# Optimization experiments

Measured on AMD Instinct MI355X. Metric: run time of the kernel, lower is better.

## Reference

```python
import jax, jax.numpy as jnp
import numpy as np

N = 50000      # nodes
E = 800000     # edges (avg degree 16)
D_IN = 32      # raw feature dim
D = 96         # hidden == out dim (residual requires equality)
L = 4          # number of GatedGCN layers
NC = 10        # n_classes
EPS = 1e-6


def _w(k, shape, fan_in):
    return jax.random.normal(k, shape, jnp.float32) / np.sqrt(fan_in).astype(np.float32)


def setup_inputs() -> dict:
    key = jax.random.key(0)
    ks = jax.random.split(key, 16)
    inp = {
        'h': jax.random.normal(ks[0], (N, D_IN), jnp.float32),
        'e': jax.random.normal(ks[1], (E, D_IN), jnp.float32),
        'src': jax.random.randint(ks[2], (E,), 0, N, jnp.int32),
        'dst': jax.random.randint(ks[3], (E,), 0, N, jnp.int32),
        'fp_w': _w(ks[4], (D_IN, D), D_IN), 'fp_b': jnp.zeros((D,), jnp.float32),
        'ep_w': _w(ks[5], (D_IN, D), D_IN), 'ep_b': jnp.zeros((D,), jnp.float32),
    }
    for i, name in enumerate(['A', 'B', 'C', 'D', 'E']):
        inp[name + '_w'] = _w(ks[6 + i], (L, D, D), D)
        inp[name + '_b'] = jnp.zeros((L, D), jnp.float32)
    inp['mlp0_w'] = _w(ks[11], (D, D // 2), D); inp['mlp0_b'] = jnp.zeros((D // 2,), jnp.float32)
    inp['mlp1_w'] = _w(ks[12], (D // 2, D // 4), D // 2); inp['mlp1_b'] = jnp.zeros((D // 4,), jnp.float32)
    inp['mlp2_w'] = _w(ks[13], (D // 4, NC), D // 4); inp['mlp2_b'] = jnp.zeros((NC,), jnp.float32)
    return inp


def reference(h, e, src, dst, fp_w, fp_b, ep_w, ep_b,
              A_w, A_b, B_w, B_b, C_w, C_b, D_w, D_b, E_w, E_b,
              mlp0_w, mlp0_b, mlp1_w, mlp1_b, mlp2_w, mlp2_b):
    # input projections
    h = h @ fp_w + fp_b                       # [N, D]
    e = e @ ep_w + ep_b                       # [E, D]

    def layer(carry, p):
        h, e = carry
        Aw, Ab, Bw, Bb, Cw, Cb, Dw, Db, Ew, Eb = p
        Ah = h @ Aw + Ab
        Bh = h @ Bw + Bb
        Ce = e @ Cw + Cb
        Dh = h @ Dw + Db
        Eh = h @ Ew + Eb
        # edge gate: e_ij = D h_i + E h_j + C e_ij  (u_add_v with u=src, v=dst)
        e_new = Dh[src] + Eh[dst] + Ce          # [E, D]
        sigma = jax.nn.sigmoid(e_new)           # [E, D]
        # gated aggregation to destination nodes
        num = jax.ops.segment_sum(Bh[src] * sigma, dst, num_segments=N)  # [N, D]
        den = jax.ops.segment_sum(sigma, dst, num_segments=N)            # [N, D]
        h_new = Ah + num / (den + EPS)
        # relu then residual (batch_norm=False, dropout eval no-op)
        return (h + jax.nn.relu(h_new), e + jax.nn.relu(e_new)), None

    (h, e), _ = jax.lax.scan(layer, (h, e),
                             (A_w, A_b, B_w, B_b, C_w, C_b, D_w, D_b, E_w, E_b))

    # MLPReadout (L=2 halvings) + sigmoid head
    y = jax.nn.relu(h @ mlp0_w + mlp0_b)
    y = jax.nn.relu(y @ mlp1_w + mlp1_b)
    y = y @ mlp2_w + mlp2_b
    return jax.nn.sigmoid(y)                    # [N, NC]
```

## Files before the change

kernel.cpp:

```cpp
#include <hip/hip_runtime.h>

#define NN 50000
#define NE 800000
#define DIN 32
#define DD 96
#define NL 4
#define NCLS 10
#define EPSF 1e-6f

typedef unsigned short u16;
typedef unsigned int u32;

typedef __bf16 bf16x8 __attribute__((ext_vector_type(8)));
typedef float f32x4 __attribute__((ext_vector_type(4)));

static __device__ __forceinline__ float bf2f(u16 u) {
    return __uint_as_float(((u32)u) << 16);
}
static __device__ __forceinline__ u16 f2bf(float f) {
    u32 x = __float_as_uint(f);
    x += 0x7FFFu + ((x >> 16) & 1u);
    return (u16)(x >> 16);
}
static __device__ __forceinline__ u32 pk2(float a, float b) {
    return (u32)f2bf(a) | ((u32)f2bf(b) << 16);
}
static __device__ __forceinline__ float unlo(u32 u) { return __uint_as_float(u << 16); }
static __device__ __forceinline__ float unhi(u32 u) { return __uint_as_float(u & 0xFFFF0000u); }

__global__ void k_zero_i(int* __restrict__ p, int n) {
    int i = blockIdx.x * blockDim.x + threadIdx.x;
    if (i < n) p[i] = 0;
}

__global__ void k_hist(const int* __restrict__ dst, int* __restrict__ counts) {
    int i = blockIdx.x * blockDim.x + threadIdx.x;
    if (i < NE) atomicAdd(&counts[dst[i]], 1);
}

__global__ __launch_bounds__(1024) void k_scan(const int* __restrict__ counts,
                                               int* __restrict__ row_ptr,
                                               int* __restrict__ cursor, int n) {
    __shared__ int wsum[16];
    __shared__ int carry_s;
    const int tid = threadIdx.x;
    const int lane = tid & 63, wid = tid >> 6;
    if (tid == 0) carry_s = 0;
    __syncthreads();
    for (int base = 0; base < n; base += 1024) {
        int i = base + tid;
        int v = (i < n) ? counts[i] : 0;
        int x = v;
#pragma unroll
        for (int off = 1; off < 64; off <<= 1) {
            int t = __shfl_up(x, (unsigned)off, 64);
            if (lane >= off) x += t;
        }
        if (lane == 63) wsum[wid] = x;
        __syncthreads();
        if (wid == 0 && lane < 16) {
            int s = wsum[lane];
#pragma unroll
            for (int off = 1; off < 16; off <<= 1) {
                int t = __shfl_up(s, (unsigned)off, 16);
                if (lane >= off) s += t;
            }
            wsum[lane] = s;
        }
        __syncthreads();
        int wbase = (wid > 0) ? wsum[wid - 1] : 0;
        int carry = carry_s;
        int excl = carry + wbase + x - v;
        if (i < n) { row_ptr[i] = excl; cursor[i] = excl; }
        __syncthreads();
        if (tid == 0) carry_s = carry + wsum[15];
        __syncthreads();
    }
    if (tid == 0) row_ptr[n] = carry_s;
}

__global__ void k_scatter(const int* __restrict__ src, const int* __restrict__ dst,
                          int* __restrict__ cursor, int* __restrict__ eperm,
                          int* __restrict__ srcp) {
    int i = blockIdx.x * blockDim.x + threadIdx.x;
    if (i >= NE) return;
    int pos = atomicAdd(&cursor[dst[i]], 1);
    eperm[pos] = i;
    srcp[pos] = src[i];
}

__global__ void k_packCw(const float* __restrict__ W_all, u16* __restrict__ wf, int kperm) {
    int q = blockIdx.x * blockDim.x + threadIdx.x;
    if (q >= NL * 6 * 3 * 64) return;
    int l = q / (6 * 3 * 64);
    int rem = q - l * (6 * 3 * 64);
    int tile = rem / (3 * 64);
    int rem2 = rem - tile * (3 * 64);
    int c = rem2 >> 6, lane = rem2 & 63;
    const float* W = W_all + (long)l * DD * DD;
    int n = tile * 16 + (lane & 15);
    int k0 = c * 32 + (lane >> 4) * 8;
    u16 w[8];
#pragma unroll
    for (int j = 0; j < 8; ++j) {
        int kk = k0 + j;
        int kact = kperm ? ((kk % 6) * 16 + kk / 6) : kk;
        w[j] = f2bf(W[kact * DD + n]);
    }
    *(uint4*)&wf[(long)q * 8] = *(uint4*)w;
}

__global__ void k_packW32(const float* __restrict__ W, u16* __restrict__ wf) {
    int q = blockIdx.x * blockDim.x + threadIdx.x;
    if (q >= 6 * 64) return;
    int tile = q >> 6, lane = q & 63;
    int n = tile * 16 + (lane & 15);
    int k0 = (lane >> 4) * 8;
    u16 w[8];
#pragma unroll
    for (int j = 0; j < 8; ++j) w[j] = f2bf(W[(k0 + j) * DD + n]);
    *(uint4*)&wf[q * 8] = *(uint4*)w;
}

template <bool BFOUT, bool PERM, bool POUT>
__global__ __launch_bounds__(256) void k_proj_m(const float* __restrict__ X,
                                                const u16* __restrict__ wf,
                                                const float* __restrict__ B,
                                                void* __restrict__ Y,
                                                const int* __restrict__ eperm,
                                                int ntiles) {
    const int lane = threadIdx.x & 63;
    const int gw = (blockIdx.x * blockDim.x + threadIdx.x) >> 6;
    const int nw = (gridDim.x * blockDim.x) >> 6;
    const int lm = lane & 15, quad = lane >> 4;

    bf16x8 bfr[6];
    float bias[6];
#pragma unroll
    for (int t = 0; t < 6; ++t) {
        bfr[t] = *(const bf16x8*)&wf[(t * 64 + lane) * 8];
        bias[t] = B[t * 16 + lm];
    }

    for (int tile = gw; tile < ntiles; tile += nw) {
        const int row = tile * 16 + lm;
        const long srow = PERM ? (long)eperm[row] : (long)row;
        float4 x0 = *(const float4*)&X[srow * DIN + quad * 8];
        float4 x1 = *(const float4*)&X[srow * DIN + quad * 8 + 4];
        u32 ap[4] = {pk2(x0.x, x0.y), pk2(x0.z, x0.w), pk2(x1.x, x1.y), pk2(x1.z, x1.w)};
        bf16x8 af = *(bf16x8*)ap;
        f32x4 acc[6];
#pragma unroll
        for (int t = 0; t < 6; ++t) {
            acc[t] = (f32x4){0.f, 0.f, 0.f, 0.f};
            acc[t] = __builtin_amdgcn_mfma_f32_16x16x32_bf16(af, bfr[t], acc[t], 0, 0, 0);
        }
        const long rbase = (long)tile * 16 + quad * 4;
        if (POUT) {
#pragma unroll
            for (int r = 0; r < 4; ++r) {
                u16* p = (u16*)Y + (rbase + r) * DD + lm * 6;
                *(u32*)p       = pk2(acc[0][r] + bias[0], acc[1][r] + bias[1]);
                *(u32*)(p + 2) = pk2(acc[2][r] + bias[2], acc[3][r] + bias[3]);
                *(u32*)(p + 4) = pk2(acc[4][r] + bias[4], acc[5][r] + bias[5]);
            }
        } else {
#pragma unroll
            for (int t = 0; t < 6; ++t) {
                const int j = t * 16 + lm;
#pragma unroll
                for (int r = 0; r < 4; ++r) {
                    float v = acc[t][r] + bias[t];
                    if (BFOUT) ((u16*)Y)[(rbase + r) * DD + j] = f2bf(v);
                    else       ((float*)Y)[(rbase + r) * DD + j] = v;
                }
            }
        }
    }
}

__global__ __launch_bounds__(256) void k_gemm4m(const float* __restrict__ X,
                                                const u16* __restrict__ awf, const float* __restrict__ ab,
                                                const u16* __restrict__ bwf, const float* __restrict__ bb,
                                                const u16* __restrict__ dwf, const float* __restrict__ db,
                                                const u16* __restrict__ ewf, const float* __restrict__ eb,
                                                float* __restrict__ Y0, u16* __restrict__ Y1,
                                                u16* __restrict__ Y2, u16* __restrict__ Y3,
                                                int ntiles) {
    const int lane = threadIdx.x & 63;
    const int w = threadIdx.x >> 6;
    const int lm = lane & 15, quad = lane >> 4;
    const u16* wf = (w == 0) ? awf : (w == 1) ? bwf : (w == 2) ? dwf : ewf;
    const float* bp = (w == 0) ? ab : (w == 1) ? bb : (w == 2) ? db : eb;

    bf16x8 bfr[6][3];
    float bias[6];
#pragma unroll
    for (int t = 0; t < 6; ++t) {
#pragma unroll
        for (int c = 0; c < 3; ++c)
            bfr[t][c] = *(const bf16x8*)&wf[((t * 3 + c) * 64 + lane) * 8];
        bias[t] = bp[t * 16 + lm];
    }

    for (int tile = blockIdx.x; tile < ntiles; tile += gridDim.x) {
        const float* xr = X + (long)(tile * 16 + lm) * DD;
        bf16x8 a[3];
#pragma unroll
        for (int c = 0; c < 3; ++c) {
            float4 x0 = *(const float4*)&xr[c * 32 + quad * 8];
            float4 x1 = *(const float4*)&xr[c * 32 + quad * 8 + 4];
            u32 ap[4] = {pk2(x0.x, x0.y), pk2(x0.z, x0.w), pk2(x1.x, x1.y), pk2(x1.z, x1.w)};
            a[c] = *(bf16x8*)ap;
        }
        f32x4 acc[6];
#pragma unroll
        for (int t = 0; t < 6; ++t) {
            acc[t] = (f32x4){0.f, 0.f, 0.f, 0.f};
#pragma unroll
            for (int c = 0; c < 3; ++c)
                acc[t] = __builtin_amdgcn_mfma_f32_16x16x32_bf16(a[c], bfr[t][c], acc[t], 0, 0, 0);
        }
        const long rbase = (long)tile * 16 + quad * 4;
        if (w == 0) {
#pragma unroll
            for (int t = 0; t < 6; ++t) {
                const int j = t * 16 + lm;
#pragma unroll
                for (int r = 0; r < 4; ++r) Y0[(rbase + r) * DD + j] = acc[t][r] + bias[t];
            }
        } else {
            u16* Yp = (w == 1) ? Y1 : (w == 2) ? Y2 : Y3;
#pragma unroll
            for (int r = 0; r < 4; ++r) {
                u16* p = Yp + (rbase + r) * DD + lm * 6;
                *(u32*)p       = pk2(acc[0][r] + bias[0], acc[1][r] + bias[1]);
                *(u32*)(p + 2) = pk2(acc[2][r] + bias[2], acc[3][r] + bias[3]);
                *(u32*)(p + 4) = pk2(acc[4][r] + bias[4], acc[5][r] + bias[5]);
            }
        }
    }
}

__global__ __launch_bounds__(256) void k_node_edge_w(u16* ebuf,
                                                     const u16* __restrict__ cwf,
                                                     const float* __restrict__ Cb,
                                                     const u16* __restrict__ Dh,
                                                     const u16* __restrict__ Eh,
                                                     const u16* __restrict__ Bh,
                                                     const int* __restrict__ srcp,
                                                     const int* __restrict__ row_ptr,
                                                     const float* __restrict__ Ah,
                                                     float* __restrict__ hbuf) {
    const int lane = threadIdx.x & 63;
    const int gw = (blockIdx.x * blockDim.x + threadIdx.x) >> 6;
    const int nw = (gridDim.x * blockDim.x) >> 6;
    const int lm = lane & 15, quad = lane >> 4;

    bf16x8 bfrag[6][3];
    float cb[6];
#pragma unroll
    for (int t = 0; t < 6; ++t) {
#pragma unroll
        for (int c = 0; c < 3; ++c)
            bfrag[t][c] = *(const bf16x8*)&cwf[((t * 3 + c) * 64 + lane) * 8];
        cb[t] = Cb[t * 16 + lm];
    }

    for (int n = gw; n < NN; n += nw) {
        const int r0 = row_ptr[n], r1 = row_ptr[n + 1];
        float eh[6];
        {
            const u16* ep = Eh + (long)n * DD + lm * 6;
            u32 e0 = *(const u32*)ep, e1 = *(const u32*)(ep + 2), e2 = *(const u32*)(ep + 4);
            eh[0] = unlo(e0); eh[1] = unhi(e0); eh[2] = unlo(e1);
            eh[3] = unhi(e1); eh[4] = unlo(e2); eh[5] = unhi(e2);
        }
        float nacc[6] = {0.f, 0.f, 0.f, 0.f, 0.f, 0.f};
        float dacc[6] = {0.f, 0.f, 0.f, 0.f, 0.f, 0.f};

        for (int chunk = r0; chunk < r1; chunk += 16) {
            const int rows = r1 - chunk < 16 ? r1 - chunk : 16;
            const long arow = chunk + (lm < rows ? lm : 0);
            bf16x8 a[3];
#pragma unroll
            for (int c = 0; c < 3; ++c)
                a[c] = *(const bf16x8*)&ebuf[arow * DD + c * 32 + quad * 8];
            int sr[4];
#pragma unroll
            for (int r = 0; r < 4; ++r) {
                int rl = quad * 4 + r;
                sr[r] = (chunk + rl < r1) ? srcp[chunk + rl] : 0;
            }
            f32x4 acc[6];
#pragma unroll
            for (int t = 0; t < 6; ++t) {
                acc[t] = (f32x4){0.f, 0.f, 0.f, 0.f};
#pragma unroll
                for (int c = 0; c < 3; ++c)
                    acc[t] = __builtin_amdgcn_mfma_f32_16x16x32_bf16(a[c], bfrag[t][c], acc[t], 0, 0, 0);
            }
#pragma unroll
            for (int r = 0; r < 4; ++r) {
                const int rl = quad * 4 + r;
                if (rl < rows) {
                    const long s = sr[r];
                    const u16* dp = Dh + s * DD + lm * 6;
                    const u16* bp = Bh + s * DD + lm * 6;
                    u16* ep = ebuf + (long)(chunk + rl) * DD + lm * 6;
                    u32 d0 = *(const u32*)dp, d1 = *(const u32*)(dp + 2), d2 = *(const u32*)(dp + 4);
                    u32 b0 = *(const u32*)bp, b1 = *(const u32*)(bp + 2), b2 = *(const u32*)(bp + 4);
                    u32 o0 = *(const u32*)ep, o1 = *(const u32*)(ep + 2), o2 = *(const u32*)(ep + 4);
                    float dh[6] = {unlo(d0), unhi(d0), unlo(d1), unhi(d1), unlo(d2), unhi(d2)};
                    float bh[6] = {unlo(b0), unhi(b0), unlo(b1), unhi(b1), unlo(b2), unhi(b2)};
                    float od[6] = {unlo(o0), unhi(o0), unlo(o1), unhi(o1), unlo(o2), unhi(o2)};
                    float ov[6];
#pragma unroll
                    for (int t = 0; t < 6; ++t) {
                        float en = acc[t][r] + cb[t] + dh[t] + eh[t];
                        float sg = 1.f / (1.f + __expf(-en));
                        nacc[t] += bh[t] * sg;
                        dacc[t] += sg;
                        ov[t] = od[t] + fmaxf(en, 0.f);
                    }
                    *(u32*)ep       = pk2(ov[0], ov[1]);
                    *(u32*)(ep + 2) = pk2(ov[2], ov[3]);
                    *(u32*)(ep + 4) = pk2(ov[4], ov[5]);
                }
            }
        }
#pragma unroll
        for (int t = 0; t < 6; ++t) {
            float x = nacc[t], y = dacc[t];
            x += __shfl_xor(x, 16); y += __shfl_xor(y, 16);
            x += __shfl_xor(x, 32); y += __shfl_xor(y, 32);
            nacc[t] = x; dacc[t] = y;
        }
        if (quad == 0) {
#pragma unroll
            for (int t = 0; t < 6; ++t) {
                const int j = t * 16 + lm;
                float val = Ah[(long)n * DD + j] + nacc[t] / (dacc[t] + EPSF);
                hbuf[(long)n * DD + j] += fmaxf(val, 0.f);
            }
        }
    }
}

__global__ void k_mlp(const float* __restrict__ X, const float* __restrict__ W,
                      const float* __restrict__ B, float* __restrict__ Y,
                      int K, int Dout, int act, long total) {
    long idx = (long)blockIdx.x * blockDim.x + threadIdx.x;
    if (idx >= total) return;
    int row = (int)(idx / Dout);
    int j = (int)(idx - (long)row * Dout);
    const float* xr = X + (long)row * K;
    float acc = B[j];
    for (int k = 0; k < K; ++k) acc = fmaf(xr[k], W[k * Dout + j], acc);
    if (act == 1) acc = fmaxf(acc, 0.f);
    else if (act == 2) acc = 1.f / (1.f + __expf(-acc));
    Y[idx] = acc;
}

extern "C" void kernel_launch(void* const* d_in, const int* in_sizes, int n_in,
                              void* d_out, int out_size, void* d_ws, size_t ws_size,
                              hipStream_t stream) {
    const float* h_in = (const float*)d_in[0];
    const float* e_in = (const float*)d_in[1];
    const int* src = (const int*)d_in[2];
    const int* dst = (const int*)d_in[3];
    const float* fp_w = (const float*)d_in[4];
    const float* fp_b = (const float*)d_in[5];
    const float* ep_w = (const float*)d_in[6];
    const float* ep_b = (const float*)d_in[7];
    const float* A_w = (const float*)d_in[8];
    const float* A_b = (const float*)d_in[9];
    const float* B_w = (const float*)d_in[10];
    const float* B_b = (const float*)d_in[11];
    const float* C_w = (const float*)d_in[12];
    const float* C_b = (const float*)d_in[13];
    const float* D_w = (const float*)d_in[14];
    const float* D_b = (const float*)d_in[15];
    const float* E_w = (const float*)d_in[16];
    const float* E_b = (const float*)d_in[17];
    const float* mlp0_w = (const float*)d_in[18];
    const float* mlp0_b = (const float*)d_in[19];
    const float* mlp1_w = (const float*)d_in[20];
    const float* mlp1_b = (const float*)d_in[21];
    const float* mlp2_w = (const float*)d_in[22];
    const float* mlp2_b = (const float*)d_in[23];
    float* out = (float*)d_out;

    const size_t ND = (size_t)NN * DD;
    const size_t ED = (size_t)NE * DD;
    const size_t FRAG = (size_t)NL * 6 * 3 * 64 * 8;
    char* w = (char*)d_ws;
    float* hbuf = (float*)w; w += ND * 4;
    float* Ahb  = (float*)w; w += ND * 4;
    u16* Bhb = (u16*)w; w += ND * 2;
    u16* Dhb = (u16*)w; w += ND * 2;
    u16* Ehb = (u16*)w; w += ND * 2;
    u16* ebuf = (u16*)w; w += ED * 2;
    int* counts  = (int*)w; w += (size_t)NN * 4;
    int* row_ptr = (int*)w; w += (size_t)(NN + 1) * 4 + 12;
    int* cursor  = (int*)w; w += (size_t)NN * 4;
    int* eperm   = (int*)w; w += (size_t)NE * 4;
    int* srcp    = (int*)w; w += (size_t)NE * 4;
    u16* awf = (u16*)w; w += FRAG * 2;
    u16* bwf = (u16*)w; w += FRAG * 2;
    u16* cwf = (u16*)w; w += FRAG * 2;
    u16* dwf = (u16*)w; w += FRAG * 2;
    u16* ewf = (u16*)w; w += FRAG * 2;
    u16* wfp = (u16*)w; w += (size_t)6 * 64 * 8 * 2;
    u16* wep = (u16*)w; w += (size_t)6 * 64 * 8 * 2;
    size_t need = (size_t)(w - (char*)d_ws);
    if (ws_size < need) return;

    k_zero_i<<<(NN + 255) / 256, 256, 0, stream>>>(counts, NN);
    k_hist<<<(NE + 255) / 256, 256, 0, stream>>>(dst, counts);
    k_scan<<<1, 1024, 0, stream>>>(counts, row_ptr, cursor, NN);
    k_scatter<<<(NE + 255) / 256, 256, 0, stream>>>(src, dst, cursor, eperm, srcp);
    const int gPack = (NL * 6 * 3 * 64 + 255) / 256;
    k_packCw<<<gPack, 256, 0, stream>>>(A_w, awf, 0);
    k_packCw<<<gPack, 256, 0, stream>>>(B_w, bwf, 0);
    k_packCw<<<gPack, 256, 0, stream>>>(C_w, cwf, 1);
    k_packCw<<<gPack, 256, 0, stream>>>(D_w, dwf, 0);
    k_packCw<<<gPack, 256, 0, stream>>>(E_w, ewf, 0);
    k_packW32<<<2, 256, 0, stream>>>(fp_w, wfp);
    k_packW32<<<2, 256, 0, stream>>>(ep_w, wep);

    k_proj_m<false, false, false><<<256, 256, 0, stream>>>(h_in, wfp, fp_b, hbuf, nullptr, NN / 16);
    k_proj_m<true, true, true><<<1024, 256, 0, stream>>>(e_in, wep, ep_b, ebuf, eperm, NE / 16);

    const size_t LFRAG = (size_t)6 * 3 * 64 * 8;
    for (int l = 0; l < NL; ++l) {
        const float* Ab = A_b + (size_t)l * DD;
        const float* Bb = B_b + (size_t)l * DD;
        const float* Cb = C_b + (size_t)l * DD;
        const float* Db = D_b + (size_t)l * DD;
        const float* Eb = E_b + (size_t)l * DD;

        k_gemm4m<<<640, 256, 0, stream>>>(hbuf,
                                          awf + l * LFRAG, Ab, bwf + l * LFRAG, Bb,
                                          dwf + l * LFRAG, Db, ewf + l * LFRAG, Eb,
                                          Ahb, Bhb, Dhb, Ehb, NN / 16);
        k_node_edge_w<<<2560, 256, 0, stream>>>(ebuf, cwf + l * LFRAG, Cb, Dhb, Ehb, Bhb,
                                                srcp, row_ptr, Ahb, hbuf);
    }

    float* y1 = Ahb;
    float* y2 = Ahb + (size_t)NN * 48;
    long t0 = (long)NN * 48, t1 = (long)NN * 24, t2 = (long)NN * NCLS;
    k_mlp<<<(int)((t0 + 255) / 256), 256, 0, stream>>>(hbuf, mlp0_w, mlp0_b, y1, DD, 48, 1, t0);
    k_mlp<<<(int)((t1 + 255) / 256), 256, 0, stream>>>(y1, mlp1_w, mlp1_b, y2, 48, 24, 1, t1);
    k_mlp<<<(int)((t2 + 255) / 256), 256, 0, stream>>>(y2, mlp2_w, mlp2_b, out, 24, NCLS, 2, t2);
}
```

Measured before the change: 1.430 ms.

## Split edge work into 16-edge chunks with atomic num/den accumulation

Replaces per-node wave assignment in the edge kernel with a flat list of 16-edge chunks, built once by a second scan over per-node chunk counts. This is meant to fix load imbalance from skewed node degrees. Partial numerator and denominator sums now go to zeroed fp32 buffers through atomicAdd, and a separate combine kernel applies the residual update. In exchange it adds two extra kernels and extra global traffic per layer (zeroing two N×D buffers, atomics, one more pass). The gemm4m grid is also enlarged.

```diff
diff --git a/kernel.cpp b/kernel.cpp
--- a/kernel.cpp
+++ b/kernel.cpp
@@ -33,13 +33,18 @@
     if (i < n) p[i] = 0;
 }
 
+__global__ void k_zero_f4(float4* __restrict__ p, int n4) {
+    int i = blockIdx.x * blockDim.x + threadIdx.x;
+    if (i < n4) p[i] = make_float4(0.f, 0.f, 0.f, 0.f);
+}
+
 __global__ void k_hist(const int* __restrict__ dst, int* __restrict__ counts) {
     int i = blockIdx.x * blockDim.x + threadIdx.x;
     if (i < NE) atomicAdd(&counts[dst[i]], 1);
 }
 
 __global__ __launch_bounds__(1024) void k_scan(const int* __restrict__ counts,
-                                               int* __restrict__ row_ptr,
+                                               int* __restrict__ ptr,
                                                int* __restrict__ cursor, int n) {
     __shared__ int wsum[16];
     __shared__ int carry_s;
@@ -71,12 +76,12 @@
         int wbase = (wid > 0) ? wsum[wid - 1] : 0;
         int carry = carry_s;
         int excl = carry + wbase + x - v;
-        if (i < n) { row_ptr[i] = excl; cursor[i] = excl; }
+        if (i < n) { ptr[i] = excl; cursor[i] = excl; }
         __syncthreads();
         if (tid == 0) carry_s = carry + wsum[15];
         __syncthreads();
     }
-    if (tid == 0) row_ptr[n] = carry_s;
+    if (tid == 0) ptr[n] = carry_s;
 }
 
 __global__ void k_scatter(const int* __restrict__ src, const int* __restrict__ dst,
@@ -87,6 +92,23 @@
     int pos = atomicAdd(&cursor[dst[i]], 1);
     eperm[pos] = i;
     srcp[pos] = src[i];
+}
+
+__global__ void k_chunkcnt(const int* __restrict__ row_ptr, int* __restrict__ counts) {
+    int n = blockIdx.x * blockDim.x + threadIdx.x;
+    if (n < NN) counts[n] = (row_ptr[n + 1] - row_ptr[n] + 15) / 16;
+}
+
+__global__ void k_fillchunk(const int* __restrict__ row_ptr, const int* __restrict__ chunk_ptr,
+                            int* __restrict__ chunk_node, int* __restrict__ chunk_start) {
+    int n = blockIdx.x * blockDim.x + threadIdx.x;
+    if (n >= NN) return;
+    int r0 = row_ptr[n], r1 = row_ptr[n + 1];
+    int base = chunk_ptr[n];
+    for (int c = 0; r0 + 16 * c < r1; ++c) {
+        chunk_node[base + c] = n;
+        chunk_start[base + c] = r0 + 16 * c;
+    }
 }
 
 __global__ void k_packCw(const float* __restrict__ W_all, u16* __restrict__ wf, int kperm) {
@@ -242,16 +264,19 @@
     }
 }
 
-__global__ __launch_bounds__(256) void k_node_edge_w(u16* ebuf,
-                                                     const u16* __restrict__ cwf,
-                                                     const float* __restrict__ Cb,
-                                                     const u16* __restrict__ Dh,
-                                                     const u16* __restrict__ Eh,
-                                                     const u16* __restrict__ Bh,
-                                                     const int* __restrict__ srcp,
-                                                     const int* __restrict__ row_ptr,
-                                                     const float* __restrict__ Ah,
-                                                     float* __restrict__ hbuf) {
+__global__ __launch_bounds__(256) void k_edge_c(u16* ebuf,
+                                                const u16* __restrict__ cwf,
+                                                const float* __restrict__ Cb,
+                                                const u16* __restrict__ Dh,
+                                                const u16* __restrict__ Eh,
+                                                const u16* __restrict__ Bh,
+                                                const int* __restrict__ srcp,
+                                                const int* __restrict__ row_ptr,
+                                                const int* __restrict__ chunk_node,
+                                                const int* __restrict__ chunk_start,
+                                                const int* __restrict__ chunk_total,
+                                                float* __restrict__ num,
+                                                float* __restrict__ den) {
     const int lane = threadIdx.x & 63;
     const int gw = (blockIdx.x * blockDim.x + threadIdx.x) >> 6;
     const int nw = (gridDim.x * blockDim.x) >> 6;
@@ -266,9 +291,12 @@
             bfrag[t][c] = *(const bf16x8*)&cwf[((t * 3 + c) * 64 + lane) * 8];
         cb[t] = Cb[t * 16 + lm];
     }
-
-    for (int n = gw; n < NN; n += nw) {
-        const int r0 = row_ptr[n], r1 = row_ptr[n + 1];
+    const int cnt = *chunk_total;
+
+    for (int ci = gw; ci < cnt; ci += nw) {
+        const int n = chunk_node[ci];
+        const int start = chunk_start[ci];
+        const int rows = min(16, row_ptr[n + 1] - start);
         float eh[6];
         {
             const u16* ep = Eh + (long)n * DD + lm * 6;
@@ -276,57 +304,53 @@
             eh[0] = unlo(e0); eh[1] = unhi(e0); eh[2] = unlo(e1);
             eh[3] = unhi(e1); eh[4] = unlo(e2); eh[5] = unhi(e2);
         }
+        const long arow = start + (lm < rows ? lm : 0);
+        bf16x8 a[3];
+#pragma unroll
+        for (int c = 0; c < 3; ++c)
+            a[c] = *(const bf16x8*)&ebuf[arow * DD + c * 32 + quad * 8];
+        int sr[4];
+#pragma unroll
+        for (int r = 0; r < 4; ++r) {
+            int rl = quad * 4 + r;
+            sr[r] = (rl < rows) ? srcp[start + rl] : 0;
+        }
+        f32x4 acc[6];
+#pragma unroll
+        for (int t = 0; t < 6; ++t) {
+            acc[t] = (f32x4){0.f, 0.f, 0.f, 0.f};
+#pragma unroll
+            for (int c = 0; c < 3; ++c)
+                acc[t] = __builtin_amdgcn_mfma_f32_16x16x32_bf16(a[c], bfrag[t][c], acc[t], 0, 0, 0);
+        }
         float nacc[6] = {0.f, 0.f, 0.f, 0.f, 0.f, 0.f};
         float dacc[6] = {0.f, 0.f, 0.f, 0.f, 0.f, 0.f};
-
-        for (int chunk = r0; chunk < r1; chunk += 16) {
-            const int rows = r1 - chunk < 16 ? r1 - chunk : 16;
-            const long arow = chunk + (lm < rows ? lm : 0);
-            bf16x8 a[3];
-#pragma unroll
-            for (int c = 0; c < 3; ++c)
-                a[c] = *(const bf16x8*)&ebuf[arow * DD + c * 32 + quad * 8];
-            int sr[4];
-#pragma unroll
-            for (int r = 0; r < 4; ++r) {
-                int rl = quad * 4 + r;
-                sr[r] = (chunk + rl < r1) ? srcp[chunk + rl] : 0;
-            }
-            f32x4 acc[6];
-#pragma unroll
-            for (int t = 0; t < 6; ++t) {
-                acc[t] = (f32x4){0.f, 0.f, 0.f, 0.f};
-#pragma unroll
-                for (int c = 0; c < 3; ++c)
-                    acc[t] = __builtin_amdgcn_mfma_f32_16x16x32_bf16(a[c], bfrag[t][c], acc[t], 0, 0, 0);
-            }
-#pragma unroll
-            for (int r = 0; r < 4; ++r) {
-                const int rl = quad * 4 + r;
-                if (rl < rows) {
-                    const long s = sr[r];
-                    const u16* dp = Dh + s * DD + lm * 6;
-                    const u16* bp = Bh + s * DD + lm * 6;
-                    u16* ep = ebuf + (long)(chunk + rl) * DD + lm * 6;
-                    u32 d0 = *(const u32*)dp, d1 = *(const u32*)(dp + 2), d2 = *(const u32*)(dp + 4);
-                    u32 b0 = *(const u32*)bp, b1 = *(const u32*)(bp + 2), b2 = *(const u32*)(bp + 4);
-                    u32 o0 = *(const u32*)ep, o1 = *(const u32*)(ep + 2), o2 = *(const u32*)(ep + 4);
-                    float dh[6] = {unlo(d0), unhi(d0), unlo(d1), unhi(d1), unlo(d2), unhi(d2)};
-                    float bh[6] = {unlo(b0), unhi(b0), unlo(b1), unhi(b1), unlo(b2), unhi(b2)};
-                    float od[6] = {unlo(o0), unhi(o0), unlo(o1), unhi(o1), unlo(o2), unhi(o2)};
-                    float ov[6];
-#pragma unroll
-                    for (int t = 0; t < 6; ++t) {
-                        float en = acc[t][r] + cb[t] + dh[t] + eh[t];
-                        float sg = 1.f / (1.f + __expf(-en));
-                        nacc[t] += bh[t] * sg;
-                        dacc[t] += sg;
-                        ov[t] = od[t] + fmaxf(en, 0.f);
-                    }
-                    *(u32*)ep       = pk2(ov[0], ov[1]);
-                    *(u32*)(ep + 2) = pk2(ov[2], ov[3]);
-                    *(u32*)(ep + 4) = pk2(ov[4], ov[5]);
+#pragma unroll
+        for (int r = 0; r < 4; ++r) {
+            const int rl = quad * 4 + r;
+            if (rl < rows) {
+                const long s = sr[r];
+                const u16* dp = Dh + s * DD + lm * 6;
+                const u16* bp = Bh + s * DD + lm * 6;
+                u16* ep = ebuf + (long)(start + rl) * DD + lm * 6;
+                u32 d0 = *(const u32*)dp, d1 = *(const u32*)(dp + 2), d2 = *(const u32*)(dp + 4);
+                u32 b0 = *(const u32*)bp, b1 = *(const u32*)(bp + 2), b2 = *(const u32*)(bp + 4);
+                u32 o0 = *(const u32*)ep, o1 = *(const u32*)(ep + 2), o2 = *(const u32*)(ep + 4);
+                float dh[6] = {unlo(d0), unhi(d0), unlo(d1), unhi(d1), unlo(d2), unhi(d2)};
+                float bh[6] = {unlo(b0), unhi(b0), unlo(b1), unhi(b1), unlo(b2), unhi(b2)};
+                float od[6] = {unlo(o0), unhi(o0), unlo(o1), unhi(o1), unlo(o2), unhi(o2)};
+                float ov[6];
+#pragma unroll
+                for (int t = 0; t < 6; ++t) {
+                    float en = acc[t][r] + cb[t] + dh[t] + eh[t];
+                    float sg = 1.f / (1.f + __expf(-en));
+                    nacc[t] += bh[t] * sg;
+                    dacc[t] += sg;
+                    ov[t] = od[t] + fmaxf(en, 0.f);
                 }
+                *(u32*)ep       = pk2(ov[0], ov[1]);
+                *(u32*)(ep + 2) = pk2(ov[2], ov[3]);
+                *(u32*)(ep + 4) = pk2(ov[4], ov[5]);
             }
         }
 #pragma unroll
@@ -338,13 +362,26 @@
         }
         if (quad == 0) {
 #pragma unroll
-            for (int t = 0; t < 6; ++t) {
-                const int j = t * 16 + lm;
-                float val = Ah[(long)n * DD + j] + nacc[t] / (dacc[t] + EPSF);
-                hbuf[(long)n * DD + j] += fmaxf(val, 0.f);
-            }
-        }
-    }
+            for (int t = 0; t < 6; ++t)
+                atomicAdd(&num[(long)n * DD + t * 16 + lm], nacc[t]);
+        } else if (quad == 1) {
+#pragma unroll
+            for (int t = 0; t < 6; ++t)
+                atomicAdd(&den[(long)n * DD + t * 16 + lm], dacc[t]);
+        }
+    }
+}
+
+__global__ void k_comb(const float4* __restrict__ Ah, const float4* __restrict__ num,
+                       const float4* __restrict__ den, float4* __restrict__ h, int n4) {
+    int i = blockIdx.x * blockDim.x + threadIdx.x;
+    if (i >= n4) return;
+    float4 a = Ah[i], nm = num[i], dn = den[i], hv = h[i];
+    hv.x += fmaxf(a.x + nm.x / (dn.x + EPSF), 0.f);
+    hv.y += fmaxf(a.y + nm.y / (dn.y + EPSF), 0.f);
+    hv.z += fmaxf(a.z + nm.z / (dn.z + EPSF), 0.f);
+    hv.w += fmaxf(a.w + nm.w / (dn.w + EPSF), 0.f);
+    h[i] = hv;
 }
 
 __global__ void k_mlp(const float* __restrict__ X, const float* __restrict__ W,
@@ -394,9 +431,12 @@
     const size_t ND = (size_t)NN * DD;
     const size_t ED = (size_t)NE * DD;
     const size_t FRAG = (size_t)NL * 6 * 3 * 64 * 8;
+    const int MAXCH = NN + NE / 16 + 64;
     char* w = (char*)d_ws;
     float* hbuf = (float*)w; w += ND * 4;
     float* Ahb  = (float*)w; w += ND * 4;
+    float* numb = (float*)w; w += ND * 4;
+    float* denb = (float*)w; w += ND * 4;
     u16* Bhb = (u16*)w; w += ND * 2;
     u16* Dhb = (u16*)w; w += ND * 2;
     u16* Ehb = (u16*)w; w += ND * 2;
@@ -406,6 +446,9 @@
     int* cursor  = (int*)w; w += (size_t)NN * 4;
     int* eperm   = (int*)w; w += (size_t)NE * 4;
     int* srcp    = (int*)w; w += (size_t)NE * 4;
+    int* chunk_ptr  = (int*)w; w += (size_t)(NN + 1) * 4 + 12;
+    int* chunk_node = (int*)w; w += (size_t)MAXCH * 4;
+    int* chunk_start= (int*)w; w += (size_t)MAXCH * 4;
     u16* awf = (u16*)w; w += FRAG * 2;
     u16* bwf = (u16*)w; w += FRAG * 2;
     u16* cwf = (u16*)w; w += FRAG * 2;
@@ -420,6 +463,9 @@
     k_hist<<<(NE + 255) / 256, 256, 0, stream>>>(dst, counts);
     k_scan<<<1, 1024, 0, stream>>>(counts, row_ptr, cursor, NN);
     k_scatter<<<(NE + 255) / 256, 256, 0, stream>>>(src, dst, cursor, eperm, srcp);
+    k_chunkcnt<<<(NN + 255) / 256, 256, 0, stream>>>(row_ptr, counts);
+    k_scan<<<1, 1024, 0, stream>>>(counts, chunk_ptr, cursor, NN);
+    k_fillchunk<<<(NN + 255) / 256, 256, 0, stream>>>(row_ptr, chunk_ptr, chunk_node, chunk_start);
     const int gPack = (NL * 6 * 3 * 64 + 255) / 256;
     k_packCw<<<gPack, 256, 0, stream>>>(A_w, awf, 0);
     k_packCw<<<gPack, 256, 0, stream>>>(B_w, bwf, 0);
@@ -433,6 +479,7 @@
     k_proj_m<true, true, true><<<1024, 256, 0, stream>>>(e_in, wep, ep_b, ebuf, eperm, NE / 16);
 
     const size_t LFRAG = (size_t)6 * 3 * 64 * 8;
+    const int zn4 = (int)(2 * ND / 4);
     for (int l = 0; l < NL; ++l) {
         const float* Ab = A_b + (size_t)l * DD;
         const float* Bb = B_b + (size_t)l * DD;
@@ -440,12 +487,17 @@
         const float* Db = D_b + (size_t)l * DD;
         const float* Eb = E_b + (size_t)l * DD;
 
-        k_gemm4m<<<640, 256, 0, stream>>>(hbuf,
-                                          awf + l * LFRAG, Ab, bwf + l * LFRAG, Bb,
-                                          dwf + l * LFRAG, Db, ewf + l * LFRAG, Eb,
-                                          Ahb, Bhb, Dhb, Ehb, NN / 16);
-        k_node_edge_w<<<2560, 256, 0, stream>>>(ebuf, cwf + l * LFRAG, Cb, Dhb, Ehb, Bhb,
-                                                srcp, row_ptr, Ahb, hbuf);
+        k_gemm4m<<<3125, 256, 0, stream>>>(hbuf,
+                                           awf + l * LFRAG, Ab, bwf + l * LFRAG, Bb,
+                                           dwf + l * LFRAG, Db, ewf + l * LFRAG, Eb,
+                                           Ahb, Bhb, Dhb, Ehb, NN / 16);
+        k_zero_f4<<<(zn4 + 255) / 256, 256, 0, stream>>>((float4*)numb, zn4);
+        k_edge_c<<<2560, 256, 0, stream>>>(ebuf, cwf + l * LFRAG, Cb, Dhb, Ehb, Bhb,
+                                           srcp, row_ptr, chunk_node, chunk_start,
+                                           chunk_ptr + NN, numb, denb);
+        k_comb<<<(int)((ND / 4 + 255) / 256), 256, 0, stream>>>(
+            (const float4*)Ahb, (const float4*)numb, (const float4*)denb, (float4*)hbuf,
+            (int)(ND / 4));
     }
 
     float* y1 = Ahb;
```

Result: slower. 1.549 ms (+8.3%).
